# Kernel optimization log

Measured on AMD Instinct MI355X. Metric: run time of the kernel, lower is better.

The kernel has to match this reference:

```python
import jax, jax.numpy as jnp
import numpy as np

B, C, H, W = 64, 2048, 14, 14
HID, OUT = 2048, 256
NUM_HEADS = 8
SCALE = 1.0
BN_EPS = 1e-5
NORM_EPS = 1e-12


def setup_inputs() -> dict:
    key = jax.random.key(0)
    ks = jax.random.split(key, 5)
    inp = {
        "x": jax.random.normal(ks[0], (B, C, H, W), dtype=jnp.float32),
        # proj MLP1D: conv1(k=1) -> BN -> ReLU -> conv2(k=1), bias=False
        "w1_p": jax.random.normal(ks[1], (HID, C), dtype=jnp.float32) * 0.02,
        "g_p": jnp.ones((HID,), dtype=jnp.float32),
        "b_p": jnp.zeros((HID,), dtype=jnp.float32),
        "w2_p": jax.random.normal(ks[2], (OUT, HID), dtype=jnp.float32) * 0.02,
        # proj_obj MLP1D (same structure)
        "w1_o": jax.random.normal(ks[3], (HID, C), dtype=jnp.float32) * 0.02,
        "g_o": jnp.ones((HID,), dtype=jnp.float32),
        "b_o": jnp.zeros((HID,), dtype=jnp.float32),
        "w2_o": jax.random.normal(ks[4], (OUT, HID), dtype=jnp.float32) * 0.02,
    }
    return inp


def _mlp1d(x, w1, gamma, beta, w2):
    # x: [b, c_in, L]; 1x1 conv == channel matmul
    h = jnp.einsum('oc,bcl->bol', w1, x)  # [b, HID, L]
    # BatchNorm1d, training mode: stats over (batch, length) per channel
    mu = jnp.mean(h, axis=(0, 2), keepdims=True)
    var = jnp.mean(jnp.square(h - mu), axis=(0, 2), keepdims=True)
    h = (h - mu) * jax.lax.rsqrt(var + BN_EPS)
    h = h * gamma[None, :, None] + beta[None, :, None]
    h = jax.nn.relu(h)
    return jnp.einsum('oc,bcl->bol', w2, h)  # [b, OUT, L]


def reference(x, w1_p, g_p, b_p, w2_p, w1_o, g_o, b_o, w2_o):
    b, c, h, w = x.shape
    L = h * w
    xf = x.reshape(b, c, L)                       # [b, c, L]
    x_pool = jnp.mean(xf, axis=2, keepdims=True)  # adaptive_avg_pool2d(1)
    z = _mlp1d(jnp.concatenate([x_pool, xf], axis=2), w1_p, g_p, b_p, w2_p)  # [b, OUT, L+1]
    z_g = z[:, :, :1]          # [b, OUT, 1]
    z_feat = z[:, :, 1:]       # [b, OUT, L]
    # L2 normalize over channel dim, then scale
    nrm = jnp.sqrt(jnp.sum(jnp.square(z_feat), axis=1, keepdims=True))
    a = z_feat / jnp.maximum(nrm, NORM_EPS) / SCALE
    a = a.reshape(b, NUM_HEADS, -1, L)            # [b, H, K, L], K = OUT/H
    obj_attn_raw = jax.nn.softmax(a, axis=-1)
    obj_attn = obj_attn_raw                        # group branch: same softmax
    xh = xf.reshape(b, NUM_HEADS, c // NUM_HEADS, L)
    # matmul(x, attn^T): [b,H,Ch,L] x [b,H,K,L] -> [b,H,Ch,K]
    obj_val = jnp.einsum('bhcl,bhkl->bhck', xh, obj_attn)
    obj_val = obj_val.reshape(b, c, obj_attn.shape[2])  # [b, c, K]
    obj_val = _mlp1d(obj_val, w1_o, g_o, b_o, w2_o)      # [b, OUT, K]
    return (z_g, obj_val, obj_attn, obj_attn_raw)
```

## Files before the change

kernel.cpp:

```cpp
#include <hip/hip_runtime.h>
#include <hip/hip_bf16.h>
#include <math.h>

typedef __bf16 bf16;
typedef bf16 bf16x8 __attribute__((ext_vector_type(8)));
typedef float f32x4 __attribute__((ext_vector_type(4)));

constexpr int BATCH = 64;
constexpr int CIN   = 2048;
constexpr int HIDN  = 2048;
constexpr int OUTN  = 256;
constexpr int LL    = 196;
constexpr int LCAT  = 197;
constexpr int P1V   = BATCH * LCAT;
constexpr int P1P   = 12672;
constexpr size_t O_ZG   = 0;
constexpr size_t O_OVAL = (size_t)BATCH * OUTN;
constexpr size_t O_ATT  = O_OVAL + (size_t)BATCH * OUTN * 32;
constexpr size_t O_ATTR = O_ATT + (size_t)BATCH * OUTN * LL;

constexpr size_t WS_XCAT = 0;
constexpr size_t WS_V2   = WS_XCAT;
constexpr size_t WS_H2T  = WS_XCAT + (size_t)(16u<<20);
constexpr size_t WS_HT   = 51904512;
constexpr size_t WS_Z    = WS_HT + 51904512;
constexpr size_t WS_W1B  = WS_Z + 12976128;
constexpr size_t WS_W2B  = WS_W1B + 8388608;
constexpr size_t WS_W1OB = WS_W2B + 1048576;
constexpr size_t WS_W2OB = WS_W1OB + 8388608;
constexpr size_t WS_NRM  = WS_W2OB + 1048576;
constexpr size_t WS_SUMS = WS_NRM + 50176;
constexpr size_t WS_SC1  = WS_SUMS + 32768;
constexpr size_t WS_SH1  = WS_SC1 + 8192;
constexpr size_t WS_SC2  = WS_SH1 + 8192;
constexpr size_t WS_SH2  = WS_SC2 + 8192;

__device__ __forceinline__ void gload16(const bf16* g, bf16* l){
  __builtin_amdgcn_global_load_lds((const __attribute__((address_space(1))) void*)g,
                                   (__attribute__((address_space(3))) void*)l, 16, 0, 0);
}

__global__ __launch_bounds__(256) void cast_k(const float* __restrict__ s, bf16* __restrict__ d, int n){
  int i = blockIdx.x * 256 + threadIdx.x;
  if (i < n) d[i] = (bf16)s[i];
}
__global__ __launch_bounds__(256) void zero_f32(float* p, int n){
  int i = blockIdx.x * 256 + threadIdx.x;
  if (i < n) p[i] = 0.f;
}
__global__ __launch_bounds__(256) void zero_b16(bf16* p, int n){
  int i = blockIdx.x * 256 + threadIdx.x;
  if (i < n) p[i] = (bf16)0.f;
}

__global__ __launch_bounds__(256) void prep_k(const float* __restrict__ x, bf16* __restrict__ xcat){
  __shared__ float xs[64][201];
  int b  = blockIdx.x >> 5;
  int cg = blockIdx.x & 31;
  int c0 = cg * 64;
  int t  = threadIdx.x;
  const float* xb = x + ((size_t)b * CIN + c0) * LL;
  #pragma unroll
  for (int i = 0; i < 16; i++){
    int idx = i * 256 + t;
    int cc = idx >> 6, q = idx & 63;
    if (q < 49){
      float4 v = *(const float4*)(xb + (size_t)cc * LL + q * 4);
      xs[cc][q*4+0] = v.x; xs[cc][q*4+1] = v.y; xs[cc][q*4+2] = v.z; xs[cc][q*4+3] = v.w;
    }
  }
  __syncthreads();
  if (t < 64){
    float s = 0.f;
    for (int l = 0; l < LL; l++) s += xs[t][l];
    xcat[(size_t)(b * LCAT) * CIN + c0 + t] = (bf16)(s * (1.f / (float)LL));
  }
  int lw = t >> 6, cc = t & 63;
  for (int i = 0; i < 49; i++){
    int l = i * 4 + lw;
    xcat[(size_t)(b * LCAT + 1 + l) * CIN + c0 + cc] = (bf16)xs[cc][l];
  }
}

__global__ __launch_bounds__(256) void stats_k(const bf16* __restrict__ src, int rows, int rpg,
                                               float* __restrict__ sum, float* __restrict__ sumsq){
  int o  = threadIdx.x * 8;
  int r0 = blockIdx.x * rpg;
  int r1 = min(rows, r0 + rpg);
  float s[8] = {0.f,0.f,0.f,0.f,0.f,0.f,0.f,0.f};
  float q[8] = {0.f,0.f,0.f,0.f,0.f,0.f,0.f,0.f};
  for (int r = r0; r < r1; r++){
    bf16x8 v = *(const bf16x8*)(src + (size_t)r * 2048 + o);
    #pragma unroll
    for (int j = 0; j < 8; j++){ float f = (float)v[j]; s[j] += f; q[j] += f * f; }
  }
  #pragma unroll
  for (int j = 0; j < 8; j++){
    atomicAdd(&sum[o + j], s[j]);
    atomicAdd(&sumsq[o + j], q[j]);
  }
}

__global__ __launch_bounds__(256) void finalize_k(const float* __restrict__ sum, const float* __restrict__ sumsq,
                                                  const float* __restrict__ g, const float* __restrict__ b,
                                                  float n, float* __restrict__ scale, float* __restrict__ shift){
  int o = blockIdx.x * 256 + threadIdx.x;
  float mu  = sum[o] / n;
  float var = sumsq[o] / n - mu * mu;
  float sc  = g[o] / sqrtf(var + 1e-5f);
  scale[o] = sc;
  shift[o] = b[o] - mu * sc;
}

__global__ __launch_bounds__(256) void zg_k(const float* __restrict__ z, float* __restrict__ dout){
  int gidx = blockIdx.x * 256 + threadIdx.x;
  int b = gidx >> 8, c = gidx & 255;
  dout[O_ZG + gidx] = z[(size_t)c * P1P + b * LCAT];
}

__global__ __launch_bounds__(256) void nrm_k(const float* __restrict__ z, float* __restrict__ nrm){
  int b = blockIdx.x, t = threadIdx.x;
  if (t >= LL) return;
  float acc = 0.f;
  const float* zb = z + (size_t)b * LCAT + 1 + t;
  for (int c = 0; c < OUTN; c++){
    float v = zb[(size_t)c * P1P];
    acc += v * v;
  }
  nrm[b * LL + t] = sqrtf(acc);
}

__global__ __launch_bounds__(64) void softmax_k(const float* __restrict__ z, const float* __restrict__ nrm,
                                                float* __restrict__ dout){
  int bc = blockIdx.x;
  int b  = bc >> 8;
  int lane = threadIdx.x;
  const float* zr = z + (size_t)(bc & 255) * P1P + b * LCAT + 1;
  const float* nr = nrm + b * LL;
  float a[4];
  float mx = -1e30f;
  #pragma unroll
  for (int j = 0; j < 4; j++){
    int l = lane + j * 64;
    if (l < LL){
      float v = zr[l] / fmaxf(nr[l], 1e-12f);
      a[j] = v; mx = fmaxf(mx, v);
    } else a[j] = -1e30f;
  }
  #pragma unroll
  for (int s = 1; s < 64; s <<= 1) mx = fmaxf(mx, __shfl_xor(mx, s, 64));
  float sum = 0.f;
  #pragma unroll
  for (int j = 0; j < 4; j++){
    a[j] = (a[j] > -1e29f) ? expf(a[j] - mx) : 0.f;
    sum += a[j];
  }
  #pragma unroll
  for (int s = 1; s < 64; s <<= 1) sum += __shfl_xor(sum, s, 64);
  float inv = 1.f / sum;
  float* o1 = dout + O_ATT  + (size_t)bc * LL;
  float* o2 = dout + O_ATTR + (size_t)bc * LL;
  #pragma unroll
  for (int j = 0; j < 4; j++){
    int l = lane + j * 64;
    if (l < LL){ float r = a[j] * inv; o1[l] = r; o2[l] = r; }
  }
}

template<int CFG>
__global__ __launch_bounds__(256)
void gemm_k(const void* __restrict__ Ap, const void* __restrict__ Qp, void* __restrict__ Cp,
            const float* __restrict__ sc, const float* __restrict__ sh)
{
  constexpr int BM  = (CFG==5) ? 32 : (CFG==4 ? 64 : 128);
  constexpr int BN  = (CFG==5) ? 256 : (CFG==4 ? 64 : 128);
  constexpr int WR  = (CFG==5) ? 1 : 2;
  constexpr int WC  = 4 / WR;
  constexpr int WTM = BM / WR, WTN = BN / WC;
  constexpr int FM  = WTM / 16, FN = WTN / 16;
  constexpr int KT  = (CFG==5) ? 4 : 32;
  constexpr bool F32S = (CFG==5);
  constexpr bool QBN  = (CFG==2) || (CFG==4);
  constexpr bool AGL  = !F32S;
  constexpr bool QGL  = (CFG==1) || (CFG==3);
  constexpr int LDA = F32S ? LL : 2048;
  constexpr int LDQ = F32S ? LL : 2048;
  constexpr int CA  = BM / 32;
  constexpr int CQ  = BN / 32;

  __shared__ bf16 Ps[BM * 64];
  __shared__ bf16 Qs[BN * 64];

  const int t = threadIdx.x;
  const int lane = t & 63;
  const int wid  = t >> 6;
  const int wr = wid / WC, wc = wid % WC;
  const int sw8 = ((lane & 7) ^ (lane >> 3)) * 8;

  size_t aBase = 0, qBase = 0;
  int mOff = 0, nOff = 0;
  if constexpr (CFG == 5){
    int bh = blockIdx.x;
    aBase = (size_t)bh * 32 * LL;
    qBase = ((size_t)(bh >> 3) * 2048 + (size_t)(bh & 7) * 256) * LL;
    mOff = (bh >> 3) * 32;
    nOff = (bh & 7) * 256;
  } else if constexpr (CFG == 1){
    int bid = blockIdx.x;
    int wg = (bid & 7) * 198 + (bid >> 3);
    mOff = (wg >> 4) * BM;  nOff = (wg & 15) * BN;
    aBase = (size_t)mOff * LDA; qBase = (size_t)nOff * LDQ;
  } else if constexpr (CFG == 3){
    int bid = blockIdx.x;
    int wg = (bid & 7) * 32 + (bid >> 3);
    mOff = (wg >> 4) * BM;  nOff = (wg & 15) * BN;
    aBase = (size_t)mOff * LDA; qBase = (size_t)nOff * LDQ;
  } else {
    mOff = blockIdx.x * BM;
    nOff = blockIdx.y * BN;
    aBase = (size_t)mOff * LDA;
    qBase = (size_t)nOff * LDQ;
  }

  f32x4 acc[FM][FN] = {};

  for (int kt = 0; kt < KT; ++kt){
    const int k0 = kt * 64;
    bf16x8 ra[CA], rq[CQ];
    if constexpr (!AGL){
      #pragma unroll
      for (int i = 0; i < CA; i++){
        int ch = i * 256 + t;
        int row = ch >> 3, kc = ch & 7, kg = k0 + kc * 8;
        const float* g = (const float*)Ap + aBase + (size_t)row * LDA + kg;
        #pragma unroll
        for (int jj = 0; jj < 8; jj += 4){
          if (kg + jj + 3 < LL){
            float4 v = *(const float4*)(g + jj);
            ra[i][jj] = (bf16)v.x; ra[i][jj+1] = (bf16)v.y;
            ra[i][jj+2] = (bf16)v.z; ra[i][jj+3] = (bf16)v.w;
          } else {
            for (int j = jj; j < jj + 4; j++) ra[i][j] = (bf16)((kg + j) < LL ? g[j] : 0.f);
          }
        }
      }
    }
    if constexpr (!QGL){
      #pragma unroll
      for (int i = 0; i < CQ; i++){
        int ch = i * 256 + t;
        int row = ch >> 3, kc = ch & 7, kg = k0 + kc * 8;
        if constexpr (F32S){
          const float* g = (const float*)Qp + qBase + (size_t)row * LDQ + kg;
          #pragma unroll
          for (int jj = 0; jj < 8; jj += 4){
            if (kg + jj + 3 < LL){
              float4 v = *(const float4*)(g + jj);
              rq[i][jj] = (bf16)v.x; rq[i][jj+1] = (bf16)v.y;
              rq[i][jj+2] = (bf16)v.z; rq[i][jj+3] = (bf16)v.w;
            } else {
              for (int j = jj; j < jj + 4; j++) rq[i][j] = (bf16)((kg + j) < LL ? g[j] : 0.f);
            }
          }
        } else {
          bf16x8 raw = *(const bf16x8*)((const bf16*)Qp + qBase + (size_t)row * LDQ + kg);
          #pragma unroll
          for (int j = 0; j < 8; j++){
            float f = (float)raw[j] * sc[kg + j] + sh[kg + j];
            rq[i][j] = (bf16)fmaxf(f, 0.f);
          }
        }
      }
    }
    __syncthreads();
    if constexpr (AGL){
      #pragma unroll
      for (int c = 0; c < CA; c++){
        int chunk = wid * CA + c;
        int row = chunk * 8 + (lane >> 3);
        gload16((const bf16*)Ap + aBase + (size_t)row * LDA + k0 + sw8, &Ps[chunk * 512]);
      }
    }
    if constexpr (QGL){
      #pragma unroll
      for (int c = 0; c < CQ; c++){
        int chunk = wid * CQ + c;
        int row = chunk * 8 + (lane >> 3);
        gload16((const bf16*)Qp + qBase + (size_t)row * LDQ + k0 + sw8, &Qs[chunk * 512]);
      }
    }
    if constexpr (!AGL){
      #pragma unroll
      for (int i = 0; i < CA; i++){
        int ch = i * 256 + t; int row = ch >> 3, kc = ch & 7;
        *(bf16x8*)&Ps[row * 64 + ((kc ^ (row & 7)) << 3)] = ra[i];
      }
    }
    if constexpr (!QGL){
      #pragma unroll
      for (int i = 0; i < CQ; i++){
        int ch = i * 256 + t; int row = ch >> 3, kc = ch & 7;
        *(bf16x8*)&Qs[row * 64 + ((kc ^ (row & 7)) << 3)] = rq[i];
      }
    }
    __syncthreads();
    #pragma unroll
    for (int ks = 0; ks < 2; ++ks){
      const int kcl = ks * 4 + (lane >> 4);
      bf16x8 af[FM], qf[FN];
      #pragma unroll
      for (int m = 0; m < FM; m++){
        int row = wr * WTM + m * 16 + (lane & 15);
        af[m] = *(const bf16x8*)&Ps[row * 64 + ((kcl ^ (row & 7)) << 3)];
      }
      #pragma unroll
      for (int n = 0; n < FN; n++){
        int row = wc * WTN + n * 16 + (lane & 15);
        qf[n] = *(const bf16x8*)&Qs[row * 64 + ((kcl ^ (row & 7)) << 3)];
      }
      #pragma unroll
      for (int m = 0; m < FM; m++)
        #pragma unroll
        for (int n = 0; n < FN; n++)
          acc[m][n] = __builtin_amdgcn_mfma_f32_16x16x32_bf16(af[m], qf[n], acc[m][n], 0, 0, 0);
    }
  }

  #pragma unroll
  for (int m = 0; m < FM; m++){
    #pragma unroll
    for (int n = 0; n < FN; n++){
      #pragma unroll
      for (int r = 0; r < 4; r++){
        int row = mOff + wr * WTM + m * 16 + (lane >> 4) * 4 + r;
        int col = nOff + wc * WTN + n * 16 + (lane & 15);
        float v = acc[m][n][r];
        if constexpr (CFG == 1 || CFG == 3 || CFG == 5){
          ((bf16*)Cp)[(size_t)row * 2048 + col] = (bf16)v;
        } else if constexpr (CFG == 2){
          ((float*)Cp)[(size_t)row * P1P + col] = v;
        } else {
          ((float*)Cp)[O_OVAL + (size_t)(col >> 5) * 8192 + (size_t)row * 32 + (col & 31)] = v;
        }
      }
    }
  }
}

extern "C" void kernel_launch(void* const* d_in, const int* in_sizes, int n_in,
                              void* d_out, int out_size, void* d_ws, size_t ws_size,
                              hipStream_t stream){
  const float* x   = (const float*)d_in[0];
  const float* w1p = (const float*)d_in[1];
  const float* gp  = (const float*)d_in[2];
  const float* bp  = (const float*)d_in[3];
  const float* w2p = (const float*)d_in[4];
  const float* w1o = (const float*)d_in[5];
  const float* go  = (const float*)d_in[6];
  const float* bo  = (const float*)d_in[7];
  const float* w2o = (const float*)d_in[8];
  float* out = (float*)d_out;
  char* ws = (char*)d_ws;

  bf16* xcat = (bf16*)(ws + WS_XCAT);
  bf16* v2   = (bf16*)(ws + WS_V2);
  bf16* h2t  = (bf16*)(ws + WS_H2T);
  bf16* hT   = (bf16*)(ws + WS_HT);
  float* z   = (float*)(ws + WS_Z);
  bf16* w1b  = (bf16*)(ws + WS_W1B);
  bf16* w2b  = (bf16*)(ws + WS_W2B);
  bf16* w1ob = (bf16*)(ws + WS_W1OB);
  bf16* w2ob = (bf16*)(ws + WS_W2OB);
  float* nrmw = (float*)(ws + WS_NRM);
  float* sums = (float*)(ws + WS_SUMS);
  float* sc1 = (float*)(ws + WS_SC1);
  float* sh1 = (float*)(ws + WS_SH1);
  float* sc2 = (float*)(ws + WS_SC2);
  float* sh2 = (float*)(ws + WS_SH2);

  cast_k<<<16384, 256, 0, stream>>>(w1p, w1b, HIDN * CIN);
  cast_k<<<2048,  256, 0, stream>>>(w2p, w2b, OUTN * HIDN);
  cast_k<<<16384, 256, 0, stream>>>(w1o, w1ob, HIDN * CIN);
  cast_k<<<2048,  256, 0, stream>>>(w2o, w2ob, OUTN * HIDN);
  zero_f32<<<32, 256, 0, stream>>>(sums, 4 * 2048);
  zero_b16<<<512, 256, 0, stream>>>(xcat + (size_t)P1V * 2048, (P1P - P1V) * 2048);
  prep_k<<<2048, 256, 0, stream>>>(x, xcat);

  gemm_k<1><<<1584, 256, 0, stream>>>(xcat, w1b, hT, nullptr, nullptr);
  stats_k<<<32, 256, 0, stream>>>(hT, P1V, 394, sums, sums + 2048);
  finalize_k<<<8, 256, 0, stream>>>(sums, sums + 2048, gp, bp, (float)P1V, sc1, sh1);
  gemm_k<2><<<dim3(2, 99), 256, 0, stream>>>(w2b, hT, z, sc1, sh1);

  zg_k<<<64, 256, 0, stream>>>(z, out);
  nrm_k<<<64, 256, 0, stream>>>(z, nrmw);
  softmax_k<<<16384, 64, 0, stream>>>(z, nrmw, out);

  gemm_k<5><<<512, 256, 0, stream>>>(out + O_ATT, x, v2, nullptr, nullptr);
  gemm_k<3><<<256, 256, 0, stream>>>(v2, w1ob, h2t, nullptr, nullptr);
  stats_k<<<8, 256, 0, stream>>>(h2t, 2048, 256, sums + 4096, sums + 6144);
  finalize_k<<<8, 256, 0, stream>>>(sums + 4096, sums + 6144, go, bo, 2048.f, sc2, sh2);
  gemm_k<4><<<dim3(4, 32), 256, 0, stream>>>(w2ob, h2t, out, sc2, sh2);
}
```

Baseline: 730.5 us.

## Replace atomic BN stats with per-block partials and vectorize prep stores

BatchNorm statistics are now written as per-block partial sums into a workspace buffer, and the finalize kernel reduces them, replacing float atomics and the zeroing kernel. The first stats pass uses 256 blocks instead of 32 for more parallelism over the 12608-row activation. The prep kernel also writes xcat rows as 8-wide bf16 vector stores instead of scalar stores. The cost is a serial loop over up to 256 partials in finalize and extra workspace traffic.

```diff
diff --git a/kernel.cpp b/kernel.cpp
--- a/kernel.cpp
+++ b/kernel.cpp
@@ -22,6 +22,7 @@
 constexpr size_t WS_XCAT = 0;
 constexpr size_t WS_V2   = WS_XCAT;
 constexpr size_t WS_H2T  = WS_XCAT + (size_t)(16u<<20);
+constexpr size_t WS_PART = WS_XCAT + (size_t)(28u<<20);
 constexpr size_t WS_HT   = 51904512;
 constexpr size_t WS_Z    = WS_HT + 51904512;
 constexpr size_t WS_W1B  = WS_Z + 12976128;
@@ -29,8 +30,7 @@
 constexpr size_t WS_W1OB = WS_W2B + 1048576;
 constexpr size_t WS_W2OB = WS_W1OB + 8388608;
 constexpr size_t WS_NRM  = WS_W2OB + 1048576;
-constexpr size_t WS_SUMS = WS_NRM + 50176;
-constexpr size_t WS_SC1  = WS_SUMS + 32768;
+constexpr size_t WS_SC1  = WS_NRM + 50176;
 constexpr size_t WS_SH1  = WS_SC1 + 8192;
 constexpr size_t WS_SC2  = WS_SH1 + 8192;
 constexpr size_t WS_SH2  = WS_SC2 + 8192;
@@ -43,10 +43,6 @@
 __global__ __launch_bounds__(256) void cast_k(const float* __restrict__ s, bf16* __restrict__ d, int n){
   int i = blockIdx.x * 256 + threadIdx.x;
   if (i < n) d[i] = (bf16)s[i];
-}
-__global__ __launch_bounds__(256) void zero_f32(float* p, int n){
-  int i = blockIdx.x * 256 + threadIdx.x;
-  if (i < n) p[i] = 0.f;
 }
 __global__ __launch_bounds__(256) void zero_b16(bf16* p, int n){
   int i = blockIdx.x * 256 + threadIdx.x;
@@ -75,15 +71,21 @@
     for (int l = 0; l < LL; l++) s += xs[t][l];
     xcat[(size_t)(b * LCAT) * CIN + c0 + t] = (bf16)(s * (1.f / (float)LL));
   }
-  int lw = t >> 6, cc = t & 63;
-  for (int i = 0; i < 49; i++){
-    int l = i * 4 + lw;
-    xcat[(size_t)(b * LCAT + 1 + l) * CIN + c0 + cc] = (bf16)xs[cc][l];
-  }
-}
-
-__global__ __launch_bounds__(256) void stats_k(const bf16* __restrict__ src, int rows, int rpg,
-                                               float* __restrict__ sum, float* __restrict__ sumsq){
+  int lw = t >> 3, cg8 = t & 7;
+  #pragma unroll
+  for (int pass = 0; pass < 7; pass++){
+    int l = pass * 32 + lw;
+    if (l < LL){
+      bf16x8 w;
+      #pragma unroll
+      for (int j = 0; j < 8; j++) w[j] = (bf16)xs[cg8 * 8 + j][l];
+      *(bf16x8*)(xcat + (size_t)(b * LCAT + 1 + l) * CIN + c0 + cg8 * 8) = w;
+    }
+  }
+}
+
+__global__ __launch_bounds__(256) void stats_part_k(const bf16* __restrict__ src, int rows, int rpg,
+                                                    float* __restrict__ part){
   int o  = threadIdx.x * 8;
   int r0 = blockIdx.x * rpg;
   int r1 = min(rows, r0 + rpg);
@@ -94,19 +96,22 @@
     #pragma unroll
     for (int j = 0; j < 8; j++){ float f = (float)v[j]; s[j] += f; q[j] += f * f; }
   }
-  #pragma unroll
-  for (int j = 0; j < 8; j++){
-    atomicAdd(&sum[o + j], s[j]);
-    atomicAdd(&sumsq[o + j], q[j]);
-  }
-}
-
-__global__ __launch_bounds__(256) void finalize_k(const float* __restrict__ sum, const float* __restrict__ sumsq,
+  float* p = part + (size_t)blockIdx.x * 4096;
+  #pragma unroll
+  for (int j = 0; j < 8; j++){ p[o + j] = s[j]; p[2048 + o + j] = q[j]; }
+}
+
+__global__ __launch_bounds__(256) void finalize_k(const float* __restrict__ part, int np,
                                                   const float* __restrict__ g, const float* __restrict__ b,
                                                   float n, float* __restrict__ scale, float* __restrict__ shift){
   int o = blockIdx.x * 256 + threadIdx.x;
-  float mu  = sum[o] / n;
-  float var = sumsq[o] / n - mu * mu;
+  float s = 0.f, q = 0.f;
+  for (int p = 0; p < np; p++){
+    s += part[(size_t)p * 4096 + o];
+    q += part[(size_t)p * 4096 + 2048 + o];
+  }
+  float mu  = s / n;
+  float var = q / n - mu * mu;
   float sc  = g[o] / sqrtf(var + 1e-5f);
   scale[o] = sc;
   shift[o] = b[o] - mu * sc;
@@ -365,6 +370,7 @@
   bf16* xcat = (bf16*)(ws + WS_XCAT);
   bf16* v2   = (bf16*)(ws + WS_V2);
   bf16* h2t  = (bf16*)(ws + WS_H2T);
+  float* part = (float*)(ws + WS_PART);
   bf16* hT   = (bf16*)(ws + WS_HT);
   float* z   = (float*)(ws + WS_Z);
   bf16* w1b  = (bf16*)(ws + WS_W1B);
@@ -372,7 +378,6 @@
   bf16* w1ob = (bf16*)(ws + WS_W1OB);
   bf16* w2ob = (bf16*)(ws + WS_W2OB);
   float* nrmw = (float*)(ws + WS_NRM);
-  float* sums = (float*)(ws + WS_SUMS);
   float* sc1 = (float*)(ws + WS_SC1);
   float* sh1 = (float*)(ws + WS_SH1);
   float* sc2 = (float*)(ws + WS_SC2);
@@ -382,13 +387,12 @@
   cast_k<<<2048,  256, 0, stream>>>(w2p, w2b, OUTN * HIDN);
   cast_k<<<16384, 256, 0, stream>>>(w1o, w1ob, HIDN * CIN);
   cast_k<<<2048,  256, 0, stream>>>(w2o, w2ob, OUTN * HIDN);
-  zero_f32<<<32, 256, 0, stream>>>(sums, 4 * 2048);
   zero_b16<<<512, 256, 0, stream>>>(xcat + (size_t)P1V * 2048, (P1P - P1V) * 2048);
   prep_k<<<2048, 256, 0, stream>>>(x, xcat);
 
   gemm_k<1><<<1584, 256, 0, stream>>>(xcat, w1b, hT, nullptr, nullptr);
-  stats_k<<<32, 256, 0, stream>>>(hT, P1V, 394, sums, sums + 2048);
-  finalize_k<<<8, 256, 0, stream>>>(sums, sums + 2048, gp, bp, (float)P1V, sc1, sh1);
+  stats_part_k<<<256, 256, 0, stream>>>(hT, P1V, 50, part);
+  finalize_k<<<8, 256, 0, stream>>>(part, 256, gp, bp, (float)P1V, sc1, sh1);
   gemm_k<2><<<dim3(2, 99), 256, 0, stream>>>(w2b, hT, z, sc1, sh1);
 
   zg_k<<<64, 256, 0, stream>>>(z, out);
@@ -397,7 +401,7 @@
 
   gemm_k<5><<<512, 256, 0, stream>>>(out + O_ATT, x, v2, nullptr, nullptr);
   gemm_k<3><<<256, 256, 0, stream>>>(v2, w1ob, h2t, nullptr, nullptr);
-  stats_k<<<8, 256, 0, stream>>>(h2t, 2048, 256, sums + 4096, sums + 6144);
-  finalize_k<<<8, 256, 0, stream>>>(sums + 4096, sums + 6144, go, bo, 2048.f, sc2, sh2);
+  stats_part_k<<<64, 256, 0, stream>>>(h2t, 2048, 32, part);
+  finalize_k<<<8, 256, 0, stream>>>(part, 64, go, bo, 2048.f, sc2, sh2);
   gemm_k<4><<<dim3(4, 32), 256, 0, stream>>>(w2ob, h2t, out, sc2, sh2);
 }
```

Result: faster. 673.2 us (-7.9%).
